# Kernel optimization log

Measured on AMD Instinct MI355X. Metric: run time of the kernel, lower is better.

The kernel has to match this reference:

```python
import jax, jax.numpy as jnp
import numpy as np

B, S, D = 2, 2048, 2048
H = 1024          # per-expert swiglu hidden
E = 16            # num_experts
K = 2             # top_k
T = B * S
CAP = (K * T) // E  # capacity = top_k * tokens / experts * capacity_factor(1.0) = 512


def setup_inputs() -> dict:
    key = jax.random.key(0)
    ks = jax.random.split(key, 10)
    s = 0.02
    return {
        "hidden_states": jax.random.normal(ks[0], (B, S, D), jnp.float32),
        "gate_w": jax.random.normal(ks[1], (D, E), jnp.float32) * s,
        "w1": jax.random.normal(ks[2], (E, D, H), jnp.float32) * s,
        "w3": jax.random.normal(ks[3], (E, D, H), jnp.float32) * s,
        "w2": jax.random.normal(ks[4], (E, H, D), jnp.float32) * s,
        "sw1": jax.random.normal(ks[5], (D, H), jnp.float32) * s,
        "sw3": jax.random.normal(ks[6], (D, H), jnp.float32) * s,
        "sw2": jax.random.normal(ks[7], (H, D), jnp.float32) * s,
        "coef_w": jax.random.normal(ks[8], (D, 2), jnp.float32) * s,
        "coef_b": jnp.zeros((2,), jnp.float32),
    }


def _topk_gating(logits):
    """GShard-style top-k capacity gating. logits: [T,E] (gate runs in fp32).
    Returns combine [T,E,C], dispatch [T,E,C], l_aux scalar, exp_counts [E]."""
    probs = jax.nn.softmax(logits, axis=-1)                     # [T,E]
    top_vals, top_idx = jax.lax.top_k(probs, K)                 # [T,K]
    gates = top_vals / jnp.sum(top_vals, -1, keepdims=True)     # renormalize top-k
    masks = jax.nn.one_hot(top_idx, E, dtype=probs.dtype)       # [T,K,E]

    prior = jnp.zeros((E,), probs.dtype)
    combine = jnp.zeros((T, E, CAP), probs.dtype)
    for kk in range(K):  # fixed tiny K, structurally distinct slots
        m = masks[:, kk]                                        # [T,E]
        loc = jnp.cumsum(m, axis=0) - m + prior                 # position in expert buffer
        prior = prior + jnp.sum(m, axis=0)
        keep = m * (loc < CAP)                                  # capacity drop
        pos = jnp.sum(loc * m, axis=1).astype(jnp.int32)        # [T]
        loc_oh = jax.nn.one_hot(pos, CAP, dtype=probs.dtype)    # [T,C]
        combine = combine + gates[:, kk, None, None] * keep[:, :, None] * loc_oh[:, None, :]
    dispatch = (combine > 0).astype(probs.dtype)

    # load-balancing aux loss over top-1 assignment (GShard/DeepSpeed convention)
    me = jnp.mean(probs, axis=0)                                # [E]
    ce = jnp.mean(masks[:, 0], axis=0)                          # [E]
    l_aux = jnp.sum(me * ce) * E
    exp_counts = jnp.sum(masks, axis=(0, 1)).astype(jnp.int32)  # tokens routed per expert
    return combine, dispatch, l_aux, exp_counts


def _swiglu(x, a, b, c):
    return (jax.nn.silu(x @ a) * (x @ b)) @ c


def reference(hidden_states, gate_w, w1, w3, w2, sw1, sw3, sw2, coef_w, coef_b):
    x = hidden_states.reshape(T, D)
    logits = (x.astype(jnp.float32) @ gate_w)                   # gate kept in fp32
    combine, dispatch, l_aux, exp_counts = _topk_gating(logits)

    # dispatch -> grouped expert swiglu -> combine
    xe = jnp.einsum('tec,td->ecd', dispatch.astype(x.dtype), x)         # [E,C,D]
    h = jax.nn.silu(jnp.einsum('ecd,edh->ech', xe, w1)) * jnp.einsum('ecd,edh->ech', xe, w3)
    ye = jnp.einsum('ech,ehd->ecd', h, w2)                              # [E,C,D]
    moe_out = jnp.einsum('tec,ecd->td', combine.astype(x.dtype), ye)    # [T,D]

    # shared-expert residual MLP + softmax coefficient combine
    mlp_out = _swiglu(x, sw1, sw3, sw2)                                 # [T,D]
    coef = jax.nn.softmax(x @ coef_w + coef_b, axis=-1)                 # [T,2]
    out = moe_out * coef[:, 0:1] + mlp_out * coef[:, 1:2]
    return out.reshape(B, S, D), l_aux, exp_counts
```

## Files before the change

kernel.cpp:

```cpp
#include <hip/hip_runtime.h>
#include <hip/hip_bf16.h>
#include <stdint.h>

#define T_TOK 4096
#define DIM   2048
#define HID   1024
#define NE    16
#define CAPE  512

typedef __bf16 bf16x8 __attribute__((ext_vector_type(8)));
typedef float  f32x4  __attribute__((ext_vector_type(4)));

__device__ __forceinline__ ushort f2bf(float f) {
    union { float f; uint32_t u; } v; v.f = f;
    uint32_t r = (v.u + 0x7FFFu + ((v.u >> 16) & 1u)) >> 16;
    return (ushort)r;
}
__device__ __forceinline__ float bf2f(ushort u) {
    union { uint32_t u; float f; } v; v.u = (uint32_t)u << 16; return v.f;
}
__device__ __forceinline__ void gload16(const void* g, void* lds) {
    __builtin_amdgcn_global_load_lds(
        (const __attribute__((address_space(1))) uint32_t*)g,
        (__attribute__((address_space(3))) uint32_t*)lds, 16, 0, 0);
}
#define VMCNT(n) asm volatile("s_waitcnt vmcnt(" #n ")" ::: "memory")

__global__ __launch_bounds__(256) void logits_kernel(
    const float* __restrict__ x, const float* __restrict__ gate_w,
    const float* __restrict__ coef_w, float* __restrict__ logits,
    ushort* __restrict__ xb)
{
    int t = blockIdx.x * 4 + (threadIdx.x >> 6);
    int lane = threadIdx.x & 63;
    const float* xr = x + (size_t)t * DIM;
    float acc[18];
#pragma unroll
    for (int o = 0; o < 18; ++o) acc[o] = 0.f;
#pragma unroll
    for (int g = 0; g < DIM / 512; ++g) {
        int d = g * 512 + lane * 8;
        float4 a = *(const float4*)(xr + d);
        float4 b4 = *(const float4*)(xr + d + 4);
        float xv[8] = {a.x, a.y, a.z, a.w, b4.x, b4.y, b4.z, b4.w};
        ushort ob[8];
#pragma unroll
        for (int j = 0; j < 8; ++j) {
            const float* gw = gate_w + (size_t)(d + j) * NE;
#pragma unroll
            for (int o = 0; o < NE; ++o) acc[o] += xv[j] * gw[o];
            acc[16] += xv[j] * coef_w[(d + j) * 2 + 0];
            acc[17] += xv[j] * coef_w[(d + j) * 2 + 1];
            ob[j] = f2bf(xv[j]);
        }
        *(uint4*)(xb + (size_t)t * DIM + d) = *(uint4*)ob;
    }
#pragma unroll
    for (int off = 32; off > 0; off >>= 1) {
#pragma unroll
        for (int o = 0; o < 18; ++o) acc[o] += __shfl_down(acc[o], off, 64);
    }
    if (lane == 0) {
#pragma unroll
        for (int o = 0; o < 18; ++o) logits[(size_t)t * 18 + o] = acc[o];
    }
}

__global__ __launch_bounds__(256) void finish_kernel(
    const float* __restrict__ logits, const float* __restrict__ coef_b,
    int* __restrict__ topidx, float* __restrict__ gatesw,
    float* __restrict__ coefo, float* __restrict__ probs_part,
    float* __restrict__ laux)
{
    __shared__ float wred[4][NE];
    int t = blockIdx.x * 256 + threadIdx.x;
    float lg[18];
#pragma unroll
    for (int o = 0; o < 18; ++o) lg[o] = logits[(size_t)t * 18 + o];
    float p[NE];
    float m = lg[0];
#pragma unroll
    for (int e = 1; e < NE; ++e) m = fmaxf(m, lg[e]);
    float ssum = 0.f;
#pragma unroll
    for (int e = 0; e < NE; ++e) { p[e] = expf(lg[e] - m); ssum += p[e]; }
    float inv = 1.f / ssum;
#pragma unroll
    for (int e = 0; e < NE; ++e) p[e] *= inv;
    int i1 = 0;
#pragma unroll
    for (int e = 1; e < NE; ++e) if (p[e] > p[i1]) i1 = e;
    int i2 = -1;
#pragma unroll
    for (int e = 0; e < NE; ++e) { if (e == i1) continue; if (i2 < 0 || p[e] > p[i2]) i2 = e; }
    float g0 = p[i1], g1 = p[i2], gs = g0 + g1;
    topidx[t * 2 + 0] = i1; topidx[t * 2 + 1] = i2;
    gatesw[t * 2 + 0] = g0 / gs; gatesw[t * 2 + 1] = g1 / gs;
    float c0 = lg[16] + coef_b[0], c1 = lg[17] + coef_b[1];
    float cm = fmaxf(c0, c1);
    float e0 = expf(c0 - cm), e1 = expf(c1 - cm);
    float cs = e0 + e1;
    coefo[t * 2 + 0] = e0 / cs; coefo[t * 2 + 1] = e1 / cs;

    float r[NE];
#pragma unroll
    for (int e = 0; e < NE; ++e) r[e] = p[e];
#pragma unroll
    for (int off = 32; off > 0; off >>= 1) {
#pragma unroll
        for (int e = 0; e < NE; ++e) r[e] += __shfl_down(r[e], off, 64);
    }
    int wv = threadIdx.x >> 6, ln = threadIdx.x & 63;
    if (ln == 0) {
#pragma unroll
        for (int e = 0; e < NE; ++e) wred[wv][e] = r[e];
    }
    __syncthreads();
    if (threadIdx.x < NE)
        probs_part[blockIdx.x * NE + threadIdx.x] =
            wred[0][threadIdx.x] + wred[1][threadIdx.x]
          + wred[2][threadIdx.x] + wred[3][threadIdx.x];
    if (blockIdx.x == 0 && threadIdx.x == 0) laux[0] = 0.f;
}

__global__ __launch_bounds__(256) void scan_transpose(
    const int* __restrict__ topidx, const float* __restrict__ gatesw,
    const float* __restrict__ probs_part,
    int* __restrict__ sidx, float* __restrict__ swt,
    int* __restrict__ assign_token, int* __restrict__ nvalid,
    float* __restrict__ out_tail,
    const float* __restrict__ w1, const float* __restrict__ w3,
    const float* __restrict__ sw1, const float* __restrict__ sw3,
    const float* __restrict__ sw2,
    ushort* __restrict__ w1T, ushort* __restrict__ w3T,
    ushort* __restrict__ sw1T, ushort* __restrict__ sw3T, ushort* __restrict__ sw2T)
{
    __shared__ __align__(16) ushort tile[128][264];
    int tid = threadIdx.x;

    if (blockIdx.x < NE) {
        __shared__ int wcnt[4];
        __shared__ float fred[4];
        __shared__ int runs;
        __shared__ int cnt0s;
        int e = blockIdx.x;
        int wv = tid >> 6, ln = tid & 63;
        unsigned long long ltmask = (1ull << ln) - 1ull;
        if (tid == 0) runs = 0;
        __syncthreads();
        for (int kk = 0; kk < 2; ++kk) {
            for (int c = 0; c < T_TOK; c += 256) {
                int t = c + tid;
                bool m = (topidx[t * 2 + kk] == e);
                unsigned long long b = __ballot(m);
                int within = __popcll(b & ltmask);
                if (ln == 0) wcnt[wv] = __popcll(b);
                __syncthreads();
                int cross = 0;
                for (int w = 0; w < wv; ++w) cross += wcnt[w];
                int pos = runs + cross + within;
                if (m) {
                    bool keep = pos < CAPE;
                    sidx[t * 2 + kk] = keep ? (e * CAPE + pos) : -1;
                    swt[t * 2 + kk] = keep ? gatesw[t * 2 + kk] : 0.f;
                    if (keep) assign_token[e * CAPE + pos] = t;
                }
                __syncthreads();
                if (tid == 0) runs += wcnt[0] + wcnt[1] + wcnt[2] + wcnt[3];
                __syncthreads();
            }
            if (kk == 0 && tid == 0) cnt0s = runs;
            __syncthreads();
        }
        for (int p = runs + tid; p < CAPE; p += 256)
            assign_token[e * CAPE + p] = 0;
        float val = (tid < 16) ? probs_part[tid * NE + e] : 0.f;
#pragma unroll
        for (int off = 32; off > 0; off >>= 1) val += __shfl_down(val, off, 64);
        if (ln == 0) fred[wv] = val;
        __syncthreads();
        if (tid == 0) {
            float psum = fred[0] + fred[1] + fred[2] + fred[3];
            int total = runs;
            nvalid[e] = min(CAPE, total);
            out_tail[1 + e] = (float)total;
            float term = (psum / (float)T_TOK) * ((float)cnt0s / (float)T_TOK) * (float)NE;
            atomicAdd(&out_tail[0], term);
        }
        return;
    }

    int id = blockIdx.x - NE;
    const float* in; ushort* outp; int R, C, tx, ty;
    if (id < 2048) {
        int seg = id >> 10;
        int rem = id & 1023;
        int e = rem >> 6;
        int r2 = rem & 63;
        R = DIM; C = HID; tx = r2 & 7; ty = r2 >> 3;
        in   = (seg ? w3 : w1) + (size_t)e * DIM * HID;
        outp = (seg ? w3T : w1T) + (size_t)e * HID * DIM;
    } else {
        int id2 = id - 2048;
        int seg = id2 >> 6;
        int r2 = id2 & 63;
        if (seg < 2) {
            R = DIM; C = HID; tx = r2 & 7; ty = r2 >> 3;
            in = seg ? sw3 : sw1; outp = seg ? sw3T : sw1T;
        } else {
            R = HID; C = DIM; tx = r2 & 3; ty = r2 >> 2;
            in = sw2; outp = sw2T;
        }
    }
    int r0 = tx * 256, c0 = ty * 128;
    int t31 = tid & 31, t8 = tid >> 5;

#pragma unroll
    for (int it = 0; it < 8; ++it) {
        int r4 = (it * 8 + t8) * 4;
        int c4 = t31 * 4;
        const float* ip = in + (size_t)(r0 + r4) * C + c0 + c4;
        float va[4][4];
        *(float4*)va[0] = *(const float4*)(ip);
        *(float4*)va[1] = *(const float4*)(ip + C);
        *(float4*)va[2] = *(const float4*)(ip + 2 * (size_t)C);
        *(float4*)va[3] = *(const float4*)(ip + 3 * (size_t)C);
#pragma unroll
        for (int j = 0; j < 4; ++j) {
            uint2 u;
            u.x = (uint32_t)f2bf(va[0][j]) | ((uint32_t)f2bf(va[1][j]) << 16);
            u.y = (uint32_t)f2bf(va[2][j]) | ((uint32_t)f2bf(va[3][j]) << 16);
            *(uint2*)&tile[c4 + j][r4] = u;
        }
    }
    __syncthreads();

#pragma unroll
    for (int it = 0; it < 16; ++it) {
        int c = it * 8 + t8;
        int k = t31 * 8;
        uint4 o = *(const uint4*)&tile[c][k];
        *(uint4*)(outp + (size_t)(c0 + c) * R + r0 + k) = o;
    }
}

__device__ __forceinline__ void stage_half_off(
    const ushort* __restrict__ G, int k0, char* region, int tid,
    size_t off0, size_t off1)
{
#pragma unroll
    for (int q = 0; q < 2; ++q) {
        int c = q * 512 + tid;
        int row = c >> 3;
        int cb = (c & 7) << 4;
        int scb = cb ^ ((row & 7) << 4);
        const ushort* src = G + (q ? off1 : off0) + k0 + (scb >> 1);
        gload16(src, region + ((c - (tid & 63)) << 4));
    }
}

__device__ __forceinline__ bf16x8 ldfrag(const char* lds, int region, int row, int cb) {
    return *(const bf16x8*)(lds + region + row * 128 + (cb ^ ((row & 7) << 4)));
}

template<int NB>
__device__ __forceinline__ void core_single(
    const ushort* __restrict__ A, const ushort* __restrict__ B,
    size_t a0, size_t a1, size_t a2, size_t a3,
    size_t b0, size_t b1, size_t b2, size_t b3,
    int K, char* lds, f32x4 (&acc)[8][NB], int tid)
{
    const int DB = 32768 + NB * 8192;
    int lane = tid & 63;
    int wid = tid >> 6;
    int wrow = wid >> 2, wcol = wid & 3;
    int l15 = lane & 15, hi = lane >> 4;

#pragma unroll
    for (int m = 0; m < 8; ++m)
#pragma unroll
        for (int n = 0; n < NB; ++n)
            acc[m][n] = (f32x4){0.f, 0.f, 0.f, 0.f};

    int nj = K >> 7;

    stage_half_off(A, 0, lds + 0,           tid, a0, a1);
    stage_half_off(A, 0, lds + 16384,       tid, a2, a3);
    stage_half_off(B, 0, lds + 32768,       tid, b0, b1);
    if (NB == 4) stage_half_off(B, 0, lds + 32768 + 16384, tid, b2, b3);
    stage_half_off(B, 64, lds + DB + 32768, tid, b0, b1);
    if (NB == 4) stage_half_off(B, 64, lds + DB + 32768 + 16384, tid, b2, b3);
    if (NB == 4) VMCNT(4); else VMCNT(2);
    __builtin_amdgcn_s_barrier();
    __builtin_amdgcn_sched_barrier(0);

    for (int j = 0; j < nj; ++j) {
        int k1 = (2 * j + 1) << 6, k2 = (2 * j + 2) << 6, k3 = (2 * j + 3) << 6;
        bool st = (j < nj - 1);
#pragma unroll
        for (int d = 0; d < 2; ++d) {
            char* LA = lds + d * DB;
            char* LB = LA + 32768;
            char* LAo = lds + (d ^ 1) * DB;
            bf16x8 bf[NB][2];
#pragma unroll
            for (int p = 0; p < 4; ++p) {
                if (p == 0) {
#pragma unroll
                    for (int n = 0; n < NB; ++n)
#pragma unroll
                        for (int ks = 0; ks < 2; ++ks)
                            bf[n][ks] = ldfrag(LB, 0, wcol * (16 * NB) + n * 16 + l15, ks * 64 + hi * 16);
                }
                bf16x8 af[2][2];
#pragma unroll
                for (int i = 0; i < 2; ++i)
#pragma unroll
                    for (int ks = 0; ks < 2; ++ks)
                        af[i][ks] = ldfrag(LA, 0, wrow * 128 + (2 * p + i) * 16 + l15, ks * 64 + hi * 16);
                if (d == 0) {
                    if (p == 0)      stage_half_off(A, k1, LAo,         tid, a0, a1);
                    else if (p == 1) stage_half_off(A, k1, LAo + 16384, tid, a2, a3);
                    else if (p == 2) { if (st) stage_half_off(B, k2, LB, tid, b0, b1); }
                    else             { if (st && NB == 4) stage_half_off(B, k2, LB + 16384, tid, b2, b3); }
                } else {
                    if (st) {
                        if (p == 0)      stage_half_off(A, k2, LAo,         tid, a0, a1);
                        else if (p == 1) stage_half_off(A, k2, LAo + 16384, tid, a2, a3);
                        else if (p == 2) stage_half_off(B, k3, LB, tid, b0, b1);
                        else             { if (NB == 4) stage_half_off(B, k3, LB + 16384, tid, b2, b3); }
                    }
                }
                __builtin_amdgcn_s_barrier();
                if (p == 3) {
                    if (d == 0) {
                        if (st) { if (NB == 4) VMCNT(4); else VMCNT(2); }
                        else    VMCNT(0);
                    } else if (st) {
                        if (NB == 4) VMCNT(4); else VMCNT(2);
                    }
                }
                asm volatile("s_waitcnt lgkmcnt(0)" ::: "memory");
                __builtin_amdgcn_sched_barrier(0);
                __builtin_amdgcn_s_setprio(1);
#pragma unroll
                for (int i = 0; i < 2; ++i)
#pragma unroll
                    for (int n = 0; n < NB; ++n)
#pragma unroll
                        for (int ks = 0; ks < 2; ++ks)
                            acc[2 * p + i][n] = __builtin_amdgcn_mfma_f32_16x16x32_bf16(
                                af[i][ks], bf[n][ks], acc[2 * p + i][n], 0, 0, 0);
                __builtin_amdgcn_s_setprio(0);
                __builtin_amdgcn_s_barrier();
                __builtin_amdgcn_sched_barrier(0);
            }
        }
    }
}

template<int NM>
__device__ __forceinline__ void core_dual(
    const ushort* __restrict__ A, const ushort* __restrict__ B1,
    const ushort* __restrict__ B3,
    size_t a0, size_t a1, size_t a2, size_t a3,
    size_t b0, size_t b1,
    int K, char* lds, f32x4 (&acc1)[8][NM], f32x4 (&acc3)[8][NM], int tid)
{
    const int DB = 32768 + NM * 16384;
    int lane = tid & 63;
    int wid = tid >> 6;
    int wrow = wid >> 2, wcol = wid & 3;
    int l15 = lane & 15, hi = lane >> 4;

#pragma unroll
    for (int m = 0; m < 8; ++m)
#pragma unroll
        for (int n = 0; n < NM; ++n) {
            acc1[m][n] = (f32x4){0.f, 0.f, 0.f, 0.f};
            acc3[m][n] = (f32x4){0.f, 0.f, 0.f, 0.f};
        }

    int nj = K >> 7;

    stage_half_off(A, 0, lds + 0,     tid, a0, a1);
    stage_half_off(A, 0, lds + 16384, tid, a2, a3);
    stage_half_off(B1, 0, lds + 32768, tid, b0, b1);
    if (NM == 2) stage_half_off(B3, 0, lds + 32768 + 16384, tid, b0, b1);
    stage_half_off(B1, 64, lds + DB + 32768, tid, b0, b1);
    if (NM == 2) stage_half_off(B3, 64, lds + DB + 32768 + 16384, tid, b0, b1);
    if (NM == 2) VMCNT(4); else VMCNT(2);
    __builtin_amdgcn_s_barrier();
    __builtin_amdgcn_sched_barrier(0);

    for (int j = 0; j < nj; ++j) {
        int k1 = (2 * j + 1) << 6, k2 = (2 * j + 2) << 6, k3 = (2 * j + 3) << 6;
        bool st = (j < nj - 1);
#pragma unroll
        for (int d = 0; d < 2; ++d) {
            char* LA = lds + d * DB;
            char* LB = LA + 32768;
            char* LAo = lds + (d ^ 1) * DB;
            bf16x8 bf1[NM][2], bf3[NM][2];
#pragma unroll
            for (int p = 0; p < 4; ++p) {
                if (p == 0) {
#pragma unroll
                    for (int n = 0; n < NM; ++n)
#pragma unroll
                        for (int ks = 0; ks < 2; ++ks) {
                            int brow = wcol * (16 * NM) + n * 16 + l15;
                            bf1[n][ks] = ldfrag(LB, 0, brow,           ks * 64 + hi * 16);
                            bf3[n][ks] = ldfrag(LB, 0, brow + NM * 64, ks * 64 + hi * 16);
                        }
                }
                bf16x8 af[2][2];
#pragma unroll
                for (int i = 0; i < 2; ++i)
#pragma unroll
                    for (int ks = 0; ks < 2; ++ks)
                        af[i][ks] = ldfrag(LA, 0, wrow * 128 + (2 * p + i) * 16 + l15, ks * 64 + hi * 16);
                if (d == 0) {
                    if (p == 0)      stage_half_off(A, k1, LAo,         tid, a0, a1);
                    else if (p == 1) stage_half_off(A, k1, LAo + 16384, tid, a2, a3);
                    else if (p == 2) { if (st) stage_half_off(B1, k2, LB, tid, b0, b1); }
                    else             { if (st && NM == 2) stage_half_off(B3, k2, LB + 16384, tid, b0, b1); }
                } else {
                    if (st) {
                        if (p == 0)      stage_half_off(A, k2, LAo,         tid, a0, a1);
                        else if (p == 1) stage_half_off(A, k2, LAo + 16384, tid, a2, a3);
                        else if (p == 2) stage_half_off(B1, k3, LB, tid, b0, b1);
                        else             { if (NM == 2) stage_half_off(B3, k3, LB + 16384, tid, b0, b1); }
                    }
                }
                __builtin_amdgcn_s_barrier();
                if (p == 3) {
                    if (d == 0) {
                        if (st) { if (NM == 2) VMCNT(4); else VMCNT(2); }
                        else    VMCNT(0);
                    } else if (st) {
                        if (NM == 2) VMCNT(4); else VMCNT(2);
                    }
                }
                asm volatile("s_waitcnt lgkmcnt(0)" ::: "memory");
                __builtin_amdgcn_sched_barrier(0);
                __builtin_amdgcn_s_setprio(1);
#pragma unroll
                for (int i = 0; i < 2; ++i)
#pragma unroll
                    for (int n = 0; n < NM; ++n)
#pragma unroll
                        for (int ks = 0; ks < 2; ++ks) {
                            acc1[2 * p + i][n] = __builtin_amdgcn_mfma_f32_16x16x32_bf16(
                                af[i][ks], bf1[n][ks], acc1[2 * p + i][n], 0, 0, 0);
                            acc3[2 * p + i][n] = __builtin_amdgcn_mfma_f32_16x16x32_bf16(
                                af[i][ks], bf3[n][ks], acc3[2 * p + i][n], 0, 0, 0);
                        }
                __builtin_amdgcn_s_setprio(0);
                __builtin_amdgcn_s_barrier();
                __builtin_amdgcn_sched_barrier(0);
            }
        }
    }
}

__global__ __launch_bounds__(512, 2) void gemm8_up(
    const ushort* __restrict__ xb,
    const ushort* __restrict__ w1T, const ushort* __restrict__ w3T,
    const ushort* __restrict__ sw1T, const ushort* __restrict__ sw3T,
    const int* __restrict__ assign_token,
    ushort* __restrict__ HH, const int* __restrict__ nvalid)
{
    __shared__ __align__(16) char lds[131072];
    int b = blockIdx.x;
    int tid = threadIdx.x;
    int rr = tid >> 3;
    int lane = tid & 63, wid = tid >> 6;
    int wrow = wid >> 2, wcol = wid & 3;

    if (b < 256) {
        int id = (b & 7) * 32 + (b >> 3);
        int e = id >> 4, rem = id & 15;
        int mt = rem >> 3, nt = rem & 7;
        int bm = mt * 256, bn = nt * 128;
        if (bm >= nvalid[e]) return;
        const int* at = assign_token + e * CAPE + bm;
        size_t a0 = (size_t)at[rr] * DIM;
        size_t a1 = (size_t)at[64 + rr] * DIM;
        size_t a2 = (size_t)at[128 + rr] * DIM;
        size_t a3 = (size_t)at[192 + rr] * DIM;
        const ushort* B1 = w1T + (size_t)e * HID * DIM;
        const ushort* B3 = w3T + (size_t)e * HID * DIM;
        size_t b0 = (size_t)(bn + rr) * DIM;
        size_t b1 = (size_t)(bn + 64 + rr) * DIM;
        f32x4 acc1[8][2], acc3[8][2];
        core_dual<2>(xb, B1, B3, a0, a1, a2, a3, b0, b1, DIM, lds, acc1, acc3, tid);
        ushort* O = HH + (size_t)e * CAPE * HID;
        int rbase = bm + wrow * 128 + (lane >> 4) * 4;
        int cbase = bn + wcol * 32 + (lane & 15);
#pragma unroll
        for (int m = 0; m < 8; ++m)
#pragma unroll
            for (int n = 0; n < 2; ++n) {
                int col = cbase + n * 16;
#pragma unroll
                for (int r = 0; r < 4; ++r) {
                    float g = acc1[m][n][r];
                    float s = g / (1.f + __expf(-g));
                    O[(size_t)(rbase + m * 16 + r) * HID + col] = f2bf(s * acc3[m][n][r]);
                }
            }
    } else {
        int b2 = b - 256;
        int id = (b2 & 7) * 32 + (b2 >> 3);
        int mt = id >> 4, nt = id & 15;
        int bm = mt * 256, bn = nt * 64;
        size_t a0 = (size_t)(bm + rr) * DIM;
        size_t a1 = (size_t)(bm + 64 + rr) * DIM;
        size_t a2 = (size_t)(bm + 128 + rr) * DIM;
        size_t a3 = (size_t)(bm + 192 + rr) * DIM;
        size_t b0 = (size_t)(bn + rr) * DIM;
        size_t b1 = (size_t)(sw3T - sw1T) + (size_t)(bn + rr) * DIM;
        f32x4 acc1[8][1], acc3[8][1];
        core_dual<1>(xb, sw1T, sw1T, a0, a1, a2, a3, b0, b1, DIM, lds, acc1, acc3, tid);
        ushort* O = HH + (size_t)NE * CAPE * HID;
        int rbase = bm + wrow * 128 + (lane >> 4) * 4;
        int col = bn + wcol * 16 + (lane & 15);
#pragma unroll
        for (int m = 0; m < 8; ++m)
#pragma unroll
            for (int r = 0; r < 4; ++r) {
                float g = acc1[m][0][r];
                float s = g / (1.f + __expf(-g));
                O[(size_t)(rbase + m * 16 + r) * HID + col] = f2bf(s * acc3[m][0][r]);
            }
    }
}

__global__ __launch_bounds__(512, 2) void gemm8_down(
    const ushort* __restrict__ HH, const float* __restrict__ w2f,
    const ushort* __restrict__ sw2T, ushort* __restrict__ ye,
    ushort* __restrict__ mlpb, const float* __restrict__ coefo,
    const int* __restrict__ nvalid)
{
    __shared__ __align__(16) char lds[131072];
    int b = blockIdx.x;
    int tid = threadIdx.x;
    int rr = tid >> 3;
    int lane = tid & 63, wid = tid >> 6;
    int wrow = wid >> 2, wcol = wid & 3;

    if (b < 256) {
        int id = (b & 7) * 32 + (b >> 3);
        int e = id >> 4, rem = id & 15;
        int mt = rem >> 3, nt = rem & 7;
        int bm = mt * 256, bn = nt * 256;
        if (bm >= nvalid[e]) return;
        const ushort* A = HH + (size_t)e * CAPE * HID;
        const float*  W = w2f + (size_t)e * HID * DIM;
        ushort* Ob = ye + (size_t)e * CAPE * DIM;
        size_t a0 = (size_t)(bm + rr) * HID;
        size_t a1 = (size_t)(bm + 64 + rr) * HID;
        size_t a2 = (size_t)(bm + 128 + rr) * HID;
        size_t a3 = (size_t)(bm + 192 + rr) * HID;
        int nq = tid & 63;
        int kb = (tid >> 6) * 8;
        int l15 = lane & 15, hi = lane >> 4;

        f32x4 acc[8][4];
#pragma unroll
        for (int m = 0; m < 8; ++m)
#pragma unroll
            for (int n = 0; n < 4; ++n)
                acc[m][n] = (f32x4){0.f, 0.f, 0.f, 0.f};

        float4 breg[8];
        stage_half_off(A, 0, lds + 0,     tid, a0, a1);
        stage_half_off(A, 0, lds + 16384, tid, a2, a3);
        {
            const float* src = W + (size_t)kb * DIM + bn + nq * 4;
#pragma unroll
            for (int kk = 0; kk < 8; ++kk)
                breg[kk] = *(const float4*)(src + (size_t)kk * DIM);
        }
        {
            char* LB = lds + 32768;
#pragma unroll
            for (int j = 0; j < 4; ++j) {
                int r = nq * 4 + j;
                ushort pk[8];
#pragma unroll
                for (int kk = 0; kk < 8; ++kk) pk[kk] = f2bf(((const float*)&breg[kk])[j]);
                int cb = (kb * 2) ^ ((r & 7) << 4);
                *(uint4*)(LB + r * 128 + cb) = *(uint4*)pk;
            }
        }
        VMCNT(0);
        __syncthreads();

        int d = 0;
        for (int t = 0; t < HID / 64; ++t) {
            bool pf = (t < HID / 64 - 1);
            char* LA = lds + d * 65536;
            char* LB = LA + 32768;
            char* LAo = lds + (d ^ 1) * 65536;
            char* LBo = LAo + 32768;
            if (pf) {
                int k0 = (t + 1) * 64;
                stage_half_off(A, k0, LAo,         tid, a0, a1);
                stage_half_off(A, k0, LAo + 16384, tid, a2, a3);
                const float* src = W + (size_t)(k0 + kb) * DIM + bn + nq * 4;
#pragma unroll
                for (int kk = 0; kk < 8; ++kk)
                    breg[kk] = *(const float4*)(src + (size_t)kk * DIM);
            }
#pragma unroll
            for (int ks = 0; ks < 2; ++ks) {
                bf16x8 af[8], bf[4];
#pragma unroll
                for (int m = 0; m < 8; ++m)
                    af[m] = ldfrag(LA, 0, wrow * 128 + m * 16 + l15, ks * 64 + hi * 16);
#pragma unroll
                for (int n = 0; n < 4; ++n)
                    bf[n] = ldfrag(LB, 0, wcol * 64 + n * 16 + l15, ks * 64 + hi * 16);
#pragma unroll
                for (int m = 0; m < 8; ++m)
#pragma unroll
                    for (int n = 0; n < 4; ++n)
                        acc[m][n] = __builtin_amdgcn_mfma_f32_16x16x32_bf16(
                            af[m], bf[n], acc[m][n], 0, 0, 0);
            }
            if (pf) {
#pragma unroll
                for (int j = 0; j < 4; ++j) {
                    int r = nq * 4 + j;
                    ushort pk[8];
#pragma unroll
                    for (int kk = 0; kk < 8; ++kk) pk[kk] = f2bf(((const float*)&breg[kk])[j]);
                    int cb = (kb * 2) ^ ((r & 7) << 4);
                    *(uint4*)(LBo + r * 128 + cb) = *(uint4*)pk;
                }
            }
            VMCNT(0);
            __syncthreads();
            d ^= 1;
        }

        int rbase = bm + wrow * 128 + (lane >> 4) * 4;
        int cbase = bn + wcol * 64 + (lane & 15);
#pragma unroll
        for (int m = 0; m < 8; ++m)
#pragma unroll
            for (int n = 0; n < 4; ++n) {
                int col = cbase + n * 16;
#pragma unroll
                for (int r = 0; r < 4; ++r)
                    Ob[(size_t)(rbase + m * 16 + r) * DIM + col] = f2bf(acc[m][n][r]);
            }
    } else {
        int b2i = b - 256;
        int id = (b2i & 7) * 32 + (b2i >> 3);
        int mt = id >> 4, nt = id & 15;
        int bm = mt * 256, bn = nt * 128;
        const ushort* A = HH + (size_t)NE * CAPE * HID;
        const ushort* B = sw2T;
        size_t a0 = (size_t)(bm + rr) * HID;
        size_t a1 = (size_t)(bm + 64 + rr) * HID;
        size_t a2 = (size_t)(bm + 128 + rr) * HID;
        size_t a3 = (size_t)(bm + 192 + rr) * HID;
        size_t b0 = (size_t)(bn + rr) * HID;
        size_t b1 = (size_t)(bn + 64 + rr) * HID;
        f32x4 acc[8][2];
        core_single<2>(A, B, a0, a1, a2, a3, b0, b1, 0, 0, HID, lds, acc, tid);
        int rbase = bm + wrow * 128 + (lane >> 4) * 4;
        int cbase = bn + wcol * 32 + (lane & 15);
#pragma unroll
        for (int m = 0; m < 8; ++m)
#pragma unroll
            for (int n = 0; n < 2; ++n) {
                int col = cbase + n * 16;
#pragma unroll
                for (int r = 0; r < 4; ++r) {
                    int row = rbase + m * 16 + r;
                    mlpb[(size_t)row * DIM + col] = f2bf(acc[m][n][r] * coefo[2 * row + 1]);
                }
            }
    }
}

__global__ __launch_bounds__(256) void combine_kernel(
    const ushort* __restrict__ ye, const ushort* __restrict__ mlpb,
    const int* __restrict__ sidx, const float* __restrict__ swt,
    const float* __restrict__ coefo, float* __restrict__ out)
{
    int idx = blockIdx.x * 256 + threadIdx.x;
    int t = idx >> 9;
    int d = (idx & 511) << 2;
    int s0 = sidx[t * 2], s1 = sidx[t * 2 + 1];
    float c0 = coefo[t * 2];
    float w0 = swt[t * 2] * c0, w1 = swt[t * 2 + 1] * c0;
    uint2 mb = *(const uint2*)(mlpb + (size_t)t * DIM + d);
    const ushort* mp = (const ushort*)&mb;
    float4 v;
    v.x = bf2f(mp[0]); v.y = bf2f(mp[1]); v.z = bf2f(mp[2]); v.w = bf2f(mp[3]);
    if (s0 >= 0) {
        uint2 y = *(const uint2*)(ye + (size_t)s0 * DIM + d);
        const ushort* yp = (const ushort*)&y;
        v.x += w0 * bf2f(yp[0]); v.y += w0 * bf2f(yp[1]);
        v.z += w0 * bf2f(yp[2]); v.w += w0 * bf2f(yp[3]);
    }
    if (s1 >= 0) {
        uint2 y = *(const uint2*)(ye + (size_t)s1 * DIM + d);
        const ushort* yp = (const ushort*)&y;
        v.x += w1 * bf2f(yp[0]); v.y += w1 * bf2f(yp[1]);
        v.z += w1 * bf2f(yp[2]); v.w += w1 * bf2f(yp[3]);
    }
    *(float4*)(out + (size_t)t * DIM + d) = v;
}

extern "C" void kernel_launch(void* const* d_in, const int* in_sizes, int n_in,
                              void* d_out, int out_size, void* d_ws, size_t ws_size,
                              hipStream_t stream)
{
    const float* x      = (const float*)d_in[0];
    const float* gate_w = (const float*)d_in[1];
    const float* w1     = (const float*)d_in[2];
    const float* w3     = (const float*)d_in[3];
    const float* w2     = (const float*)d_in[4];
    const float* sw1    = (const float*)d_in[5];
    const float* sw3    = (const float*)d_in[6];
    const float* sw2    = (const float*)d_in[7];
    const float* coef_w = (const float*)d_in[8];
    const float* coef_b = (const float*)d_in[9];
    float* out = (float*)d_out;

    char* ws = (char*)d_ws;
    size_t off = 0;
    auto alloc = [&](size_t bytes) -> void* {
        void* p = ws + off;
        off += (bytes + 255) & ~(size_t)255;
        return p;
    };
    int*    nvalid       = (int*)alloc(NE * 4);
    int*    topidx       = (int*)alloc((size_t)T_TOK * 2 * 4);
    float*  gatesw       = (float*)alloc((size_t)T_TOK * 2 * 4);
    float*  coefo        = (float*)alloc((size_t)T_TOK * 2 * 4);
    int*    sidx         = (int*)alloc((size_t)T_TOK * 2 * 4);
    float*  swt          = (float*)alloc((size_t)T_TOK * 2 * 4);
    int*    assign_token = (int*)alloc((size_t)NE * CAPE * 4);
    float*  probs_part   = (float*)alloc((size_t)16 * NE * 4);
    float*  logits       = (float*)alloc((size_t)T_TOK * 18 * 4);
    ushort* w1T  = (ushort*)alloc((size_t)NE * HID * DIM * 2);
    ushort* w3T  = (ushort*)alloc((size_t)NE * HID * DIM * 2);
    ushort* sw1T = (ushort*)alloc((size_t)HID * DIM * 2);
    ushort* sw3T = (ushort*)alloc((size_t)HID * DIM * 2);
    ushort* sw2T = (ushort*)alloc((size_t)DIM * HID * 2);
    ushort* xb   = (ushort*)alloc((size_t)T_TOK * DIM * 2);
    size_t HROWS = (size_t)NE * CAPE + T_TOK;
    ushort* HH   = (ushort*)alloc(HROWS * HID * 2);
    ushort* ye   = (ushort*)alloc((size_t)NE * CAPE * DIM * 2);
    ushort* mlpb = (ushort*)alloc((size_t)T_TOK * DIM * 2);

    float* out_tail = out + (size_t)T_TOK * DIM;

    logits_kernel<<<T_TOK / 4, 256, 0, stream>>>(x, gate_w, coef_w, logits, xb);
    finish_kernel<<<T_TOK / 256, 256, 0, stream>>>(logits, coef_b, topidx, gatesw,
                                                   coefo, probs_part, out_tail);
    scan_transpose<<<NE + 2240, 256, 0, stream>>>(
        topidx, gatesw, probs_part, sidx, swt, assign_token, nvalid, out_tail,
        w1, w3, sw1, sw3, sw2, w1T, w3T, sw1T, sw3T, sw2T);
    gemm8_up<<<512, 512, 0, stream>>>(xb, w1T, w3T, sw1T, sw3T, assign_token, HH, nvalid);
    gemm8_down<<<512, 512, 0, stream>>>(HH, w2, sw2T, ye, mlpb, coefo, nvalid);
    combine_kernel<<<(T_TOK * (DIM / 4)) / 256, 256, 0, stream>>>(
        ye, mlpb, sidx, swt, coefo, out);
}
```

Before: 355.9 us.

## Fuse fp32-to-bf16 weight conversion of up-projection weights into the up GEMM

Removes the separate transpose/convert pass that wrote bf16 transposed copies of w1, w3, sw1 and sw3. The up GEMM now reads the fp32 weights directly, converts them to bf16 in registers and writes them swizzled into LDS as double-buffered B tiles. This saves a full write and re-read of the converted weights. In exchange the GEMM loads twice as many bytes for B, stages them through registers, and swaps the finely interleaved prefetch schedule for a simpler loop that waits on a full sync each step.

```diff
diff --git a/kernel.cpp b/kernel.cpp
--- a/kernel.cpp
+++ b/kernel.cpp
@@ -129,11 +129,7 @@
     int* __restrict__ sidx, float* __restrict__ swt,
     int* __restrict__ assign_token, int* __restrict__ nvalid,
     float* __restrict__ out_tail,
-    const float* __restrict__ w1, const float* __restrict__ w3,
-    const float* __restrict__ sw1, const float* __restrict__ sw3,
-    const float* __restrict__ sw2,
-    ushort* __restrict__ w1T, ushort* __restrict__ w3T,
-    ushort* __restrict__ sw1T, ushort* __restrict__ sw3T, ushort* __restrict__ sw2T)
+    const float* __restrict__ sw2, ushort* __restrict__ sw2T)
 {
     __shared__ __align__(16) ushort tile[128][264];
     int tid = threadIdx.x;
@@ -191,27 +187,10 @@
     }
 
     int id = blockIdx.x - NE;
-    const float* in; ushort* outp; int R, C, tx, ty;
-    if (id < 2048) {
-        int seg = id >> 10;
-        int rem = id & 1023;
-        int e = rem >> 6;
-        int r2 = rem & 63;
-        R = DIM; C = HID; tx = r2 & 7; ty = r2 >> 3;
-        in   = (seg ? w3 : w1) + (size_t)e * DIM * HID;
-        outp = (seg ? w3T : w1T) + (size_t)e * HID * DIM;
-    } else {
-        int id2 = id - 2048;
-        int seg = id2 >> 6;
-        int r2 = id2 & 63;
-        if (seg < 2) {
-            R = DIM; C = HID; tx = r2 & 7; ty = r2 >> 3;
-            in = seg ? sw3 : sw1; outp = seg ? sw3T : sw1T;
-        } else {
-            R = HID; C = DIM; tx = r2 & 3; ty = r2 >> 2;
-            in = sw2; outp = sw2T;
-        }
-    }
+    int R = HID, C = DIM;
+    int tx = id & 3, ty = id >> 2;
+    const float* in = sw2;
+    ushort* outp = sw2T;
     int r0 = tx * 256, c0 = ty * 128;
     int t31 = tid & 31, t8 = tid >> 5;
 
@@ -359,115 +338,10 @@
     }
 }
 
-template<int NM>
-__device__ __forceinline__ void core_dual(
-    const ushort* __restrict__ A, const ushort* __restrict__ B1,
-    const ushort* __restrict__ B3,
-    size_t a0, size_t a1, size_t a2, size_t a3,
-    size_t b0, size_t b1,
-    int K, char* lds, f32x4 (&acc1)[8][NM], f32x4 (&acc3)[8][NM], int tid)
-{
-    const int DB = 32768 + NM * 16384;
-    int lane = tid & 63;
-    int wid = tid >> 6;
-    int wrow = wid >> 2, wcol = wid & 3;
-    int l15 = lane & 15, hi = lane >> 4;
-
-#pragma unroll
-    for (int m = 0; m < 8; ++m)
-#pragma unroll
-        for (int n = 0; n < NM; ++n) {
-            acc1[m][n] = (f32x4){0.f, 0.f, 0.f, 0.f};
-            acc3[m][n] = (f32x4){0.f, 0.f, 0.f, 0.f};
-        }
-
-    int nj = K >> 7;
-
-    stage_half_off(A, 0, lds + 0,     tid, a0, a1);
-    stage_half_off(A, 0, lds + 16384, tid, a2, a3);
-    stage_half_off(B1, 0, lds + 32768, tid, b0, b1);
-    if (NM == 2) stage_half_off(B3, 0, lds + 32768 + 16384, tid, b0, b1);
-    stage_half_off(B1, 64, lds + DB + 32768, tid, b0, b1);
-    if (NM == 2) stage_half_off(B3, 64, lds + DB + 32768 + 16384, tid, b0, b1);
-    if (NM == 2) VMCNT(4); else VMCNT(2);
-    __builtin_amdgcn_s_barrier();
-    __builtin_amdgcn_sched_barrier(0);
-
-    for (int j = 0; j < nj; ++j) {
-        int k1 = (2 * j + 1) << 6, k2 = (2 * j + 2) << 6, k3 = (2 * j + 3) << 6;
-        bool st = (j < nj - 1);
-#pragma unroll
-        for (int d = 0; d < 2; ++d) {
-            char* LA = lds + d * DB;
-            char* LB = LA + 32768;
-            char* LAo = lds + (d ^ 1) * DB;
-            bf16x8 bf1[NM][2], bf3[NM][2];
-#pragma unroll
-            for (int p = 0; p < 4; ++p) {
-                if (p == 0) {
-#pragma unroll
-                    for (int n = 0; n < NM; ++n)
-#pragma unroll
-                        for (int ks = 0; ks < 2; ++ks) {
-                            int brow = wcol * (16 * NM) + n * 16 + l15;
-                            bf1[n][ks] = ldfrag(LB, 0, brow,           ks * 64 + hi * 16);
-                            bf3[n][ks] = ldfrag(LB, 0, brow + NM * 64, ks * 64 + hi * 16);
-                        }
-                }
-                bf16x8 af[2][2];
-#pragma unroll
-                for (int i = 0; i < 2; ++i)
-#pragma unroll
-                    for (int ks = 0; ks < 2; ++ks)
-                        af[i][ks] = ldfrag(LA, 0, wrow * 128 + (2 * p + i) * 16 + l15, ks * 64 + hi * 16);
-                if (d == 0) {
-                    if (p == 0)      stage_half_off(A, k1, LAo,         tid, a0, a1);
-                    else if (p == 1) stage_half_off(A, k1, LAo + 16384, tid, a2, a3);
-                    else if (p == 2) { if (st) stage_half_off(B1, k2, LB, tid, b0, b1); }
-                    else             { if (st && NM == 2) stage_half_off(B3, k2, LB + 16384, tid, b0, b1); }
-                } else {
-                    if (st) {
-                        if (p == 0)      stage_half_off(A, k2, LAo,         tid, a0, a1);
-                        else if (p == 1) stage_half_off(A, k2, LAo + 16384, tid, a2, a3);
-                        else if (p == 2) stage_half_off(B1, k3, LB, tid, b0, b1);
-                        else             { if (NM == 2) stage_half_off(B3, k3, LB + 16384, tid, b0, b1); }
-                    }
-                }
-                __builtin_amdgcn_s_barrier();
-                if (p == 3) {
-                    if (d == 0) {
-                        if (st) { if (NM == 2) VMCNT(4); else VMCNT(2); }
-                        else    VMCNT(0);
-                    } else if (st) {
-                        if (NM == 2) VMCNT(4); else VMCNT(2);
-                    }
-                }
-                asm volatile("s_waitcnt lgkmcnt(0)" ::: "memory");
-                __builtin_amdgcn_sched_barrier(0);
-                __builtin_amdgcn_s_setprio(1);
-#pragma unroll
-                for (int i = 0; i < 2; ++i)
-#pragma unroll
-                    for (int n = 0; n < NM; ++n)
-#pragma unroll
-                        for (int ks = 0; ks < 2; ++ks) {
-                            acc1[2 * p + i][n] = __builtin_amdgcn_mfma_f32_16x16x32_bf16(
-                                af[i][ks], bf1[n][ks], acc1[2 * p + i][n], 0, 0, 0);
-                            acc3[2 * p + i][n] = __builtin_amdgcn_mfma_f32_16x16x32_bf16(
-                                af[i][ks], bf3[n][ks], acc3[2 * p + i][n], 0, 0, 0);
-                        }
-                __builtin_amdgcn_s_setprio(0);
-                __builtin_amdgcn_s_barrier();
-                __builtin_amdgcn_sched_barrier(0);
-            }
-        }
-    }
-}
-
-__global__ __launch_bounds__(512, 2) void gemm8_up(
+__global__ __launch_bounds__(512, 2) void gemm2_up(
     const ushort* __restrict__ xb,
-    const ushort* __restrict__ w1T, const ushort* __restrict__ w3T,
-    const ushort* __restrict__ sw1T, const ushort* __restrict__ sw3T,
+    const float* __restrict__ w1f, const float* __restrict__ w3f,
+    const float* __restrict__ sw1f, const float* __restrict__ sw3f,
     const int* __restrict__ assign_token,
     ushort* __restrict__ HH, const int* __restrict__ nvalid)
 {
@@ -477,6 +351,7 @@
     int rr = tid >> 3;
     int lane = tid & 63, wid = tid >> 6;
     int wrow = wid >> 2, wcol = wid & 3;
+    int l15 = lane & 15, hi = lane >> 4;
 
     if (b < 256) {
         int id = (b & 7) * 32 + (b >> 3);
@@ -489,12 +364,98 @@
         size_t a1 = (size_t)at[64 + rr] * DIM;
         size_t a2 = (size_t)at[128 + rr] * DIM;
         size_t a3 = (size_t)at[192 + rr] * DIM;
-        const ushort* B1 = w1T + (size_t)e * HID * DIM;
-        const ushort* B3 = w3T + (size_t)e * HID * DIM;
-        size_t b0 = (size_t)(bn + rr) * DIM;
-        size_t b1 = (size_t)(bn + 64 + rr) * DIM;
+        int nq = tid & 63;
+        int kb = (tid >> 6) * 8;
+        const float* Wsrc = (nq < 32)
+            ? (w1f + (size_t)e * DIM * HID + bn + nq * 4)
+            : (w3f + (size_t)e * DIM * HID + bn + (nq - 32) * 4);
+
         f32x4 acc1[8][2], acc3[8][2];
-        core_dual<2>(xb, B1, B3, a0, a1, a2, a3, b0, b1, DIM, lds, acc1, acc3, tid);
+#pragma unroll
+        for (int m = 0; m < 8; ++m)
+#pragma unroll
+            for (int n = 0; n < 2; ++n) {
+                acc1[m][n] = (f32x4){0.f, 0.f, 0.f, 0.f};
+                acc3[m][n] = (f32x4){0.f, 0.f, 0.f, 0.f};
+            }
+
+        float4 breg[8];
+        stage_half_off(xb, 0, lds + 0,     tid, a0, a1);
+        stage_half_off(xb, 0, lds + 16384, tid, a2, a3);
+        {
+            const float* src = Wsrc + (size_t)kb * HID;
+#pragma unroll
+            for (int kk = 0; kk < 8; ++kk)
+                breg[kk] = *(const float4*)(src + (size_t)kk * HID);
+        }
+        {
+            char* LB = lds + 32768;
+#pragma unroll
+            for (int j = 0; j < 4; ++j) {
+                int r = nq * 4 + j;
+                ushort pk[8];
+#pragma unroll
+                for (int kk = 0; kk < 8; ++kk) pk[kk] = f2bf(((const float*)&breg[kk])[j]);
+                int cb = (kb * 2) ^ ((r & 7) << 4);
+                *(uint4*)(LB + r * 128 + cb) = *(uint4*)pk;
+            }
+        }
+        VMCNT(0);
+        __syncthreads();
+
+        int d = 0;
+        for (int t = 0; t < DIM / 64; ++t) {
+            bool pf = (t < DIM / 64 - 1);
+            char* LA = lds + d * 65536;
+            char* LB = LA + 32768;
+            char* LAo = lds + (d ^ 1) * 65536;
+            char* LBo = LAo + 32768;
+            if (pf) {
+                int k0 = (t + 1) * 64;
+                stage_half_off(xb, k0, LAo,         tid, a0, a1);
+                stage_half_off(xb, k0, LAo + 16384, tid, a2, a3);
+                const float* src = Wsrc + (size_t)(k0 + kb) * HID;
+#pragma unroll
+                for (int kk = 0; kk < 8; ++kk)
+                    breg[kk] = *(const float4*)(src + (size_t)kk * HID);
+            }
+#pragma unroll
+            for (int ks = 0; ks < 2; ++ks) {
+                bf16x8 af[8], bf1[2], bf3[2];
+#pragma unroll
+                for (int m = 0; m < 8; ++m)
+                    af[m] = ldfrag(LA, 0, wrow * 128 + m * 16 + l15, ks * 64 + hi * 16);
+#pragma unroll
+                for (int n = 0; n < 2; ++n) {
+                    bf1[n] = ldfrag(LB, 0, wcol * 32 + n * 16 + l15,       ks * 64 + hi * 16);
+                    bf3[n] = ldfrag(LB, 0, 128 + wcol * 32 + n * 16 + l15, ks * 64 + hi * 16);
+                }
+#pragma unroll
+                for (int m = 0; m < 8; ++m)
+#pragma unroll
+                    for (int n = 0; n < 2; ++n) {
+                        acc1[m][n] = __builtin_amdgcn_mfma_f32_16x16x32_bf16(
+                            af[m], bf1[n], acc1[m][n], 0, 0, 0);
+                        acc3[m][n] = __builtin_amdgcn_mfma_f32_16x16x32_bf16(
+                            af[m], bf3[n], acc3[m][n], 0, 0, 0);
+                    }
+            }
+            if (pf) {
+#pragma unroll
+                for (int j = 0; j < 4; ++j) {
+                    int r = nq * 4 + j;
+                    ushort pk[8];
+#pragma unroll
+                    for (int kk = 0; kk < 8; ++kk) pk[kk] = f2bf(((const float*)&breg[kk])[j]);
+                    int cb = (kb * 2) ^ ((r & 7) << 4);
+                    *(uint4*)(LBo + r * 128 + cb) = *(uint4*)pk;
+                }
+            }
+            VMCNT(0);
+            __syncthreads();
+            d ^= 1;
+        }
+
         ushort* O = HH + (size_t)e * CAPE * HID;
         int rbase = bm + wrow * 128 + (lane >> 4) * 4;
         int cbase = bn + wcol * 32 + (lane & 15);
@@ -519,10 +480,91 @@
         size_t a1 = (size_t)(bm + 64 + rr) * DIM;
         size_t a2 = (size_t)(bm + 128 + rr) * DIM;
         size_t a3 = (size_t)(bm + 192 + rr) * DIM;
-        size_t b0 = (size_t)(bn + rr) * DIM;
-        size_t b1 = (size_t)(sw3T - sw1T) + (size_t)(bn + rr) * DIM;
+        int nq = tid & 31;
+        int kb = (tid >> 5) * 4;
+        const float* Wsrc = (nq < 16)
+            ? (sw1f + bn + nq * 4)
+            : (sw3f + bn + (nq - 16) * 4);
+
         f32x4 acc1[8][1], acc3[8][1];
-        core_dual<1>(xb, sw1T, sw1T, a0, a1, a2, a3, b0, b1, DIM, lds, acc1, acc3, tid);
+#pragma unroll
+        for (int m = 0; m < 8; ++m) {
+            acc1[m][0] = (f32x4){0.f, 0.f, 0.f, 0.f};
+            acc3[m][0] = (f32x4){0.f, 0.f, 0.f, 0.f};
+        }
+
+        float4 breg[4];
+        stage_half_off(xb, 0, lds + 0,     tid, a0, a1);
+        stage_half_off(xb, 0, lds + 16384, tid, a2, a3);
+        {
+            const float* src = Wsrc + (size_t)kb * HID;
+#pragma unroll
+            for (int kk = 0; kk < 4; ++kk)
+                breg[kk] = *(const float4*)(src + (size_t)kk * HID);
+        }
+        {
+            char* LB = lds + 32768;
+#pragma unroll
+            for (int j = 0; j < 4; ++j) {
+                int r = nq * 4 + j;
+                ushort pk[4];
+#pragma unroll
+                for (int kk = 0; kk < 4; ++kk) pk[kk] = f2bf(((const float*)&breg[kk])[j]);
+                int cb = (kb * 2) ^ ((r & 7) << 4);
+                *(uint2*)(LB + r * 128 + cb) = *(uint2*)pk;
+            }
+        }
+        VMCNT(0);
+        __syncthreads();
+
+        int d = 0;
+        for (int t = 0; t < DIM / 64; ++t) {
+            bool pf = (t < DIM / 64 - 1);
+            char* LA = lds + d * 65536;
+            char* LB = LA + 32768;
+            char* LAo = lds + (d ^ 1) * 65536;
+            char* LBo = LAo + 32768;
+            if (pf) {
+                int k0 = (t + 1) * 64;
+                stage_half_off(xb, k0, LAo,         tid, a0, a1);
+                stage_half_off(xb, k0, LAo + 16384, tid, a2, a3);
+                const float* src = Wsrc + (size_t)(k0 + kb) * HID;
+#pragma unroll
+                for (int kk = 0; kk < 4; ++kk)
+                    breg[kk] = *(const float4*)(src + (size_t)kk * HID);
+            }
+#pragma unroll
+            for (int ks = 0; ks < 2; ++ks) {
+                bf16x8 af[8], bf1, bf3;
+#pragma unroll
+                for (int m = 0; m < 8; ++m)
+                    af[m] = ldfrag(LA, 0, wrow * 128 + m * 16 + l15, ks * 64 + hi * 16);
+                bf1 = ldfrag(LB, 0, wcol * 16 + l15,      ks * 64 + hi * 16);
+                bf3 = ldfrag(LB, 0, 64 + wcol * 16 + l15, ks * 64 + hi * 16);
+#pragma unroll
+                for (int m = 0; m < 8; ++m) {
+                    acc1[m][0] = __builtin_amdgcn_mfma_f32_16x16x32_bf16(
+                        af[m], bf1, acc1[m][0], 0, 0, 0);
+                    acc3[m][0] = __builtin_amdgcn_mfma_f32_16x16x32_bf16(
+                        af[m], bf3, acc3[m][0], 0, 0, 0);
+                }
+            }
+            if (pf) {
+#pragma unroll
+                for (int j = 0; j < 4; ++j) {
+                    int r = nq * 4 + j;
+                    ushort pk[4];
+#pragma unroll
+                    for (int kk = 0; kk < 4; ++kk) pk[kk] = f2bf(((const float*)&breg[kk])[j]);
+                    int cb = (kb * 2) ^ ((r & 7) << 4);
+                    *(uint2*)(LBo + r * 128 + cb) = *(uint2*)pk;
+                }
+            }
+            VMCNT(0);
+            __syncthreads();
+            d ^= 1;
+        }
+
         ushort* O = HH + (size_t)NE * CAPE * HID;
         int rbase = bm + wrow * 128 + (lane >> 4) * 4;
         int col = bn + wcol * 16 + (lane & 15);
@@ -750,10 +792,6 @@
     int*    assign_token = (int*)alloc((size_t)NE * CAPE * 4);
     float*  probs_part   = (float*)alloc((size_t)16 * NE * 4);
     float*  logits       = (float*)alloc((size_t)T_TOK * 18 * 4);
-    ushort* w1T  = (ushort*)alloc((size_t)NE * HID * DIM * 2);
-    ushort* w3T  = (ushort*)alloc((size_t)NE * HID * DIM * 2);
-    ushort* sw1T = (ushort*)alloc((size_t)HID * DIM * 2);
-    ushort* sw3T = (ushort*)alloc((size_t)HID * DIM * 2);
     ushort* sw2T = (ushort*)alloc((size_t)DIM * HID * 2);
     ushort* xb   = (ushort*)alloc((size_t)T_TOK * DIM * 2);
     size_t HROWS = (size_t)NE * CAPE + T_TOK;
@@ -766,10 +804,10 @@
     logits_kernel<<<T_TOK / 4, 256, 0, stream>>>(x, gate_w, coef_w, logits, xb);
     finish_kernel<<<T_TOK / 256, 256, 0, stream>>>(logits, coef_b, topidx, gatesw,
                                                    coefo, probs_part, out_tail);
-    scan_transpose<<<NE + 2240, 256, 0, stream>>>(
+    scan_transpose<<<NE + 64, 256, 0, stream>>>(
         topidx, gatesw, probs_part, sidx, swt, assign_token, nvalid, out_tail,
-        w1, w3, sw1, sw3, sw2, w1T, w3T, sw1T, sw3T, sw2T);
-    gemm8_up<<<512, 512, 0, stream>>>(xb, w1T, w3T, sw1T, sw3T, assign_token, HH, nvalid);
+        sw2, sw2T);
+    gemm2_up<<<512, 512, 0, stream>>>(xb, w1, w3, sw1, sw3, assign_token, HH, nvalid);
     gemm8_down<<<512, 512, 0, stream>>>(HH, w2, sw2T, ye, mlpb, coefo, nvalid);
     combine_kernel<<<(T_TOK * (DIM / 4)) / 256, 256, 0, stream>>>(
         ye, mlpb, sidx, swt, coefo, out);
```

After: 355.6 us. About the same (-0.1%).
